# Kernel optimization log

Hardware: AMD Instinct MI355X
Metric: run time of the kernel (lower is better)

The kernel has to match this reference:

```python
import jax, jax.numpy as jnp
import numpy as np

N_NODES = 100000
N_EDGES = 3200000
D_FEAT = 128
HIDDEN = 16
N_CLASSES = 7


def gcn_conv(x, edge_index, edge_weight, W, b, n_nodes):
    h = x @ W  # dense projection first (Fout small)
    src, dst = edge_index[0], edge_index[1]
    # add self-loops with weight 1
    loop = jnp.arange(n_nodes, dtype=edge_index.dtype)
    src_a = jnp.concatenate([src, loop])
    dst_a = jnp.concatenate([dst, loop])
    ew_a = jnp.concatenate([edge_weight, jnp.ones((n_nodes,), dtype=x.dtype)])
    deg = jax.ops.segment_sum(ew_a, dst_a, num_segments=n_nodes)
    dinv = jnp.where(deg > 0, jax.lax.rsqrt(deg), 0.0)
    norm = dinv[src_a] * ew_a * dinv[dst_a]  # [E+N]
    msg = h[src_a] * norm[:, None]  # gather + scale
    out = jax.ops.segment_sum(msg, dst_a, num_segments=n_nodes)
    return out + b


def setup_inputs() -> dict:
    key = jax.random.key(0)
    k = jax.random.split(key, 8)
    x = jax.random.normal(k[0], (N_NODES, D_FEAT), dtype=jnp.float32)
    edge_index = jax.random.randint(k[1], (2, N_EDGES), 0, N_NODES, dtype=jnp.int64)
    edge_weight = jax.random.uniform(k[2], (N_EDGES,), dtype=jnp.float32)
    s1 = 1.0 / np.sqrt(D_FEAT)
    s2 = 1.0 / np.sqrt(HIDDEN)
    W1 = jax.random.uniform(k[3], (D_FEAT, HIDDEN), jnp.float32, -s1, s1)
    b1 = jnp.zeros((HIDDEN,), jnp.float32)
    W2 = jax.random.uniform(k[4], (HIDDEN, N_CLASSES), jnp.float32, -s2, s2)
    b2 = jnp.zeros((N_CLASSES,), jnp.float32)
    return {"x": x, "edge_index": edge_index, "edge_weight": edge_weight,
            "W1": W1, "b1": b1, "W2": W2, "b2": b2}


def reference(x, edge_index, edge_weight, W1, b1, W2, b2):
    h = jax.nn.relu(gcn_conv(x, edge_index, edge_weight, W1, b1, N_NODES))
    out = gcn_conv(h, edge_index, edge_weight, W2, b2, N_NODES)
    return jax.nn.log_softmax(out, axis=1)
```

## Files before the change

### kernel.cpp

```cpp
#include <hip/hip_runtime.h>
#include <hip/hip_fp16.h>
#include <math.h>

constexpr int NN = 100000;
constexpr int NE = 3200000;
constexpr int DF = 128;
constexpr int NH = 16;
constexpr int NC = 7;

constexpr int BN    = 128;
constexpr int NB    = (NN + BN - 1) / BN;
constexpr int CAP   = 4608;
constexpr int CHUNK = 8192;
constexpr int AB    = (NE + CHUNK - 1) / CHUNK;
constexpr int EPT   = CHUNK / 1024;
constexpr int SPT   = (CAP + 1023) / 1024;

constexpr float QS   = 32767.0f;
constexpr float QINV = 1.0f / 32767.0f;

typedef _Float16 half8 __attribute__((ext_vector_type(8)));
typedef float    f32x4 __attribute__((ext_vector_type(4)));

__global__ void k_zero(int* __restrict__ gcur) {
    int t = blockIdx.x * blockDim.x + threadIdx.x;
    if (t < NB) gcur[t] = 0;
}

__global__ void __launch_bounds__(1024)
k_append(const int* __restrict__ src,
         const int* __restrict__ dst,
         const float* __restrict__ w,
         int* __restrict__ gcur,
         uint2* __restrict__ ebuf) {
    __shared__ int hist[NB];
    __shared__ int basev[NB];
    for (int i = threadIdx.x; i < NB; i += 1024) hist[i] = 0;
    __syncthreads();
    int e0 = blockIdx.x * CHUNK;
    unsigned slo[EPT], sw[EPT];
    int sbr[EPT];
#pragma unroll
    for (int k = 0; k < EPT; ++k) {
        int e = e0 + (int)threadIdx.x + k * 1024;
        sbr[k] = -1;
        if (e < NE) {
            int d = __builtin_nontemporal_load(dst + e);
            int b = d >> 7;
            int r = atomicAdd(&hist[b], 1);
            slo[k] = ((unsigned)(d & (BN - 1)) << 17) |
                     (unsigned)__builtin_nontemporal_load(src + e);
            sw[k]  = __float_as_uint(__builtin_nontemporal_load(w + e));
            sbr[k] = (b << 14) | r;
        }
    }
    __syncthreads();
    for (int b = threadIdx.x; b < NB; b += 1024) {
        int c = hist[b];
        basev[b] = (c > 0) ? atomicAdd(&gcur[b], c) : 0;
    }
    __syncthreads();
#pragma unroll
    for (int k = 0; k < EPT; ++k) {
        if (sbr[k] >= 0) {
            int b = sbr[k] >> 14;
            int pos = basev[b] + (sbr[k] & 0x3FFF);
            if (pos < CAP) {
                uint2 v; v.x = slo[k]; v.y = sw[k];
                ebuf[(size_t)b * CAP + pos] = v;
            }
        }
    }
}

__global__ void __launch_bounds__(1024)
k_sort(const int* __restrict__ gcur,
       uint2* __restrict__ ebuf,
       int* __restrict__ rs,
       int* __restrict__ rc,
       float* __restrict__ dinv) {
    __shared__ int cursor[BN];
    __shared__ int scanS[BN];
    __shared__ int startEx[BN];
    __shared__ unsigned sorted[CAP];
    int b = blockIdx.x;
    int tid = threadIdx.x;
    int cnt = min(gcur[b], CAP);
    const uint2* eb = ebuf + (size_t)b * CAP;
    if (tid < BN) cursor[tid] = 0;
    __syncthreads();
    unsigned sval[SPT];
    int sdr[SPT];
#pragma unroll
    for (int k = 0; k < SPT; ++k) {
        int i = tid + k * 1024;
        sdr[k] = -1;
        if (i < cnt) {
            uint2 v = eb[i];
            int dl = (v.x >> 17) & (BN - 1);
            unsigned q = (unsigned)(__uint_as_float(v.y) * QS + 0.5f);
            int r = atomicAdd(&cursor[dl], 1);
            sval[k] = (v.x & 0x1FFFF) | (q << 17);
            sdr[k] = (dl << 13) | r;
        }
    }
    __syncthreads();
    if (tid < BN) scanS[tid] = cursor[tid];
    __syncthreads();
    for (int off = 1; off < BN; off <<= 1) {
        int v = (tid < BN && tid >= off) ? scanS[tid - off] : 0;
        __syncthreads();
        if (tid < BN) scanS[tid] += v;
        __syncthreads();
    }
    if (tid < BN) {
        int ex = scanS[tid] - cursor[tid];
        startEx[tid] = ex;
        int n = b * BN + tid;
        if (n < NN) { rs[n] = b * CAP * 2 + ex; rc[n] = cursor[tid]; }
    }
    __syncthreads();
#pragma unroll
    for (int k = 0; k < SPT; ++k) {
        if (sdr[k] >= 0)
            sorted[startEx[sdr[k] >> 13] + (sdr[k] & 0x1FFF)] = sval[k];
    }
    __syncthreads();
    unsigned* eb32 = (unsigned*)ebuf + (size_t)b * CAP * 2;
    for (int i = tid; i < cnt; i += 1024) eb32[i] = sorted[i];
    if (tid < BN) {
        int n = b * BN + tid;
        if (n < NN) {
            float s = 1.0f;
            int s0 = startEx[tid], c = cursor[tid];
            for (int i = 0; i < c; ++i) s += (float)(sorted[s0 + i] >> 17) * QINV;
            dinv[n] = rsqrtf(s);
        }
    }
}

__global__ void __launch_bounds__(256)
k_proj1(const float* __restrict__ x,
        const float* __restrict__ W1,
        const float* __restrict__ dinv,
        __half* __restrict__ h1p) {
    int wave = threadIdx.x >> 6;
    int lane = threadIdx.x & 63;
    int tile = blockIdx.x * 4 + wave;
    if (tile * 16 >= NN) return;
    int m    = lane & 15;
    int quad = lane >> 4;
    half8 bfrag[4];
#pragma unroll
    for (int kc = 0; kc < 4; ++kc)
#pragma unroll
        for (int j = 0; j < 8; ++j)
            bfrag[kc][j] = (_Float16)W1[(kc * 32 + quad * 8 + j) * NH + m];
    int base = tile * 16;
    const float* xr = x + (size_t)(base + m) * DF + quad * 8;
    f32x4 acc = {0.f, 0.f, 0.f, 0.f};
#pragma unroll
    for (int kc = 0; kc < 4; ++kc) {
        const float4* p = (const float4*)(xr + kc * 32);
        float4 u0 = p[0];
        float4 u1 = p[1];
        half8 afrag;
        afrag[0] = (_Float16)u0.x; afrag[1] = (_Float16)u0.y;
        afrag[2] = (_Float16)u0.z; afrag[3] = (_Float16)u0.w;
        afrag[4] = (_Float16)u1.x; afrag[5] = (_Float16)u1.y;
        afrag[6] = (_Float16)u1.z; afrag[7] = (_Float16)u1.w;
        acc = __builtin_amdgcn_mfma_f32_16x16x32_f16(afrag, bfrag[kc], acc, 0, 0, 0);
    }
    float4 d4 = *(const float4*)(dinv + base + quad * 4);
#pragma unroll
    for (int reg = 0; reg < 4; ++reg) {
        float dd = (reg == 0) ? d4.x : (reg == 1) ? d4.y : (reg == 2) ? d4.z : d4.w;
        int row = quad * 4 + reg;
        h1p[(size_t)(base + row) * 16 + m] = __float2half(acc[reg] * dd);
    }
}

__global__ void __launch_bounds__(1024)
k_agg1p(const int* __restrict__ rs,
        const int* __restrict__ rc,
        const unsigned* __restrict__ cbuf,
        const __half* __restrict__ h1p,
        const float* __restrict__ dinv,
        const float* __restrict__ b1,
        const float* __restrict__ W2,
        __half* __restrict__ h2p) {
    const __half2* hp = (const __half2*)h1p;
    int t = blockIdx.x * 1024 + threadIdx.x;
    int n = t >> 3;
    int f2 = t & 7;
    if (n >= NN) return;
    float2 g0 = __half22float2(hp[n * 8 + f2]);
    float ax = g0.x, ay = g0.y;
    int s0 = rs[n], c = rc[n];
    int i = 0;
    for (; i + 1 < c; i += 2) {
        unsigned e0 = cbuf[s0 + i];
        unsigned e1 = cbuf[s0 + i + 1];
        float2 v0 = __half22float2(hp[(e0 & 0x1FFFF) * 8 + f2]);
        float2 v1 = __half22float2(hp[(e1 & 0x1FFFF) * 8 + f2]);
        float w0 = (float)(e0 >> 17) * QINV;
        float w1 = (float)(e1 >> 17) * QINV;
        ax += w0 * v0.x + w1 * v1.x;
        ay += w0 * v0.y + w1 * v1.y;
    }
    if (i < c) {
        unsigned e0 = cbuf[s0 + i];
        float2 v0 = __half22float2(hp[(e0 & 0x1FFFF) * 8 + f2]);
        float w0 = (float)(e0 >> 17) * QINV;
        ax += w0 * v0.x;
        ay += w0 * v0.y;
    }
    float di = dinv[n];
    float hr0 = fmaxf(di * ax + b1[2 * f2], 0.0f);
    float hr1 = fmaxf(di * ay + b1[2 * f2 + 1], 0.0f);
    float p[NC];
#pragma unroll
    for (int cc = 0; cc < NC; ++cc)
        p[cc] = hr0 * W2[(2 * f2) * NC + cc] + hr1 * W2[(2 * f2 + 1) * NC + cc];
#pragma unroll
    for (int mask = 1; mask < 8; mask <<= 1) {
#pragma unroll
        for (int cc = 0; cc < NC; ++cc)
            p[cc] += __shfl_xor(p[cc], mask, 8);
    }
    float tv = 0.0f;
#pragma unroll
    for (int cc = 0; cc < NC; ++cc)
        if (f2 == cc) tv = p[cc];
    h2p[n * 8 + f2] = __float2half(di * tv);
}

__global__ void __launch_bounds__(1024)
k_agg2_lsm(const int* __restrict__ rs,
           const int* __restrict__ rc,
           const unsigned* __restrict__ cbuf,
           const __half* __restrict__ h2p,
           const float* __restrict__ dinv,
           const float* __restrict__ b2,
           float* __restrict__ out) {
    const __half2* hp = (const __half2*)h2p;
    int t = blockIdx.x * 1024 + threadIdx.x;
    int n = t >> 2;
    int c2 = t & 3;
    if (n >= NN) return;
    float2 g0 = __half22float2(hp[n * 4 + c2]);
    float ax = g0.x, ay = g0.y;
    int s0 = rs[n], c = rc[n];
    int i = 0;
    for (; i + 1 < c; i += 2) {
        unsigned e0 = cbuf[s0 + i];
        unsigned e1 = cbuf[s0 + i + 1];
        float2 v0 = __half22float2(hp[(e0 & 0x1FFFF) * 4 + c2]);
        float2 v1 = __half22float2(hp[(e1 & 0x1FFFF) * 4 + c2]);
        float w0 = (float)(e0 >> 17) * QINV;
        float w1 = (float)(e1 >> 17) * QINV;
        ax += w0 * v0.x + w1 * v1.x;
        ay += w0 * v0.y + w1 * v1.y;
    }
    if (i < c) {
        unsigned e0 = cbuf[s0 + i];
        float2 v0 = __half22float2(hp[(e0 & 0x1FFFF) * 4 + c2]);
        float w0 = (float)(e0 >> 17) * QINV;
        ax += w0 * v0.x;
        ay += w0 * v0.y;
    }
    float di = dinv[n];
    float va = di * ax + b2[2 * c2];
    float vb = (c2 < 3) ? (di * ay + b2[2 * c2 + 1]) : -1e30f;
    float m = fmaxf(va, vb);
#pragma unroll
    for (int mask = 1; mask < 4; mask <<= 1)
        m = fmaxf(m, __shfl_xor(m, mask, 4));
    float s = __expf(va - m) + ((c2 < 3) ? __expf(vb - m) : 0.0f);
#pragma unroll
    for (int mask = 1; mask < 4; mask <<= 1)
        s += __shfl_xor(s, mask, 4);
    float lse = m + __logf(s);
    out[n * NC + 2 * c2] = va - lse;
    if (c2 < 3) out[n * NC + 2 * c2 + 1] = vb - lse;
}

extern "C" void kernel_launch(void* const* d_in, const int* in_sizes, int n_in,
                              void* d_out, int out_size, void* d_ws, size_t ws_size,
                              hipStream_t stream) {
    const float* x  = (const float*)d_in[0];
    const int*   ei = (const int*)d_in[1];
    const float* ew = (const float*)d_in[2];
    const float* W1 = (const float*)d_in[3];
    const float* b1 = (const float*)d_in[4];
    const float* W2 = (const float*)d_in[5];
    const float* b2 = (const float*)d_in[6];
    float* out = (float*)d_out;

    const int* srcp = ei;
    const int* dstp = ei + NE;

    float*  ws   = (float*)d_ws;
    float*  dinv = ws;
    __half* h1p  = (__half*)(ws + 100352);
    __half* h2p  = (__half*)(ws + 900352);
    int*    gcur = (int*)(ws + 1300352);
    int*    rs   = (int*)(ws + 1301376);
    int*    rc   = (int*)(ws + 1401728);
    uint2*  ebuf = (uint2*)(ws + 1502080);
    const unsigned* cbuf = (const unsigned*)ebuf;

    auto cdiv = [](long long a, long long b) { return (int)((a + b - 1) / b); };

    k_zero<<<1, 1024, 0, stream>>>(gcur);
    k_append<<<AB, 1024, 0, stream>>>(srcp, dstp, ew, gcur, ebuf);
    k_sort<<<NB, 1024, 0, stream>>>(gcur, ebuf, rs, rc, dinv);
    k_proj1<<<cdiv(NN, 64), 256, 0, stream>>>(x, W1, dinv, h1p);
    k_agg1p<<<cdiv((long long)NN * 8, 1024), 1024, 0, stream>>>(rs, rc, cbuf, h1p, dinv, b1, W2, h2p);
    k_agg2_lsm<<<cdiv((long long)NN * 4, 1024), 1024, 0, stream>>>(rs, rc, cbuf, h2p, dinv, b2, out);
}
```

Measured before the change: 233.5 us.

## Shard edge-bucket counters into eight segments and shrink append blocks

The append stage now spreads global bucket cursors over eight segment-specific counter arrays, each with its own edge buffer, and uses smaller 256-thread blocks with 2048-edge chunks. The goal is to cut atomic contention on the shared per-bucket cursors and to raise occupancy in the append kernel. The sort kernel gathers all eight segments per bucket and writes the compacted result to a separate buffer instead of writing back in place. In exchange there are four times as many append blocks, each running a per-bucket histogram loop over all buckets. Per-segment capacity limits (640) add overflow truncation risk, and the workspace layout gets larger.

```diff
diff --git a/kernel.cpp b/kernel.cpp
--- a/kernel.cpp
+++ b/kernel.cpp
@@ -10,11 +10,13 @@
 
 constexpr int BN    = 128;
 constexpr int NB    = (NN + BN - 1) / BN;
-constexpr int CAP   = 4608;
-constexpr int CHUNK = 8192;
+constexpr int NSEG  = 8;
+constexpr int CAPS  = 640;
+constexpr int CAPC  = 4608;
+constexpr int SORTW = NSEG * CAPS;
+constexpr int CHUNK = 2048;
 constexpr int AB    = (NE + CHUNK - 1) / CHUNK;
-constexpr int EPT   = CHUNK / 1024;
-constexpr int SPT   = (CAP + 1023) / 1024;
+constexpr int EPT   = CHUNK / 256;
 
 constexpr float QS   = 32767.0f;
 constexpr float QINV = 1.0f / 32767.0f;
@@ -24,25 +26,26 @@
 
 __global__ void k_zero(int* __restrict__ gcur) {
     int t = blockIdx.x * blockDim.x + threadIdx.x;
-    if (t < NB) gcur[t] = 0;
-}
-
-__global__ void __launch_bounds__(1024)
+    if (t < NSEG * 1024) gcur[t] = 0;
+}
+
+__global__ void __launch_bounds__(256)
 k_append(const int* __restrict__ src,
          const int* __restrict__ dst,
          const float* __restrict__ w,
          int* __restrict__ gcur,
-         uint2* __restrict__ ebuf) {
+         uint2* __restrict__ ebufseg) {
     __shared__ int hist[NB];
     __shared__ int basev[NB];
-    for (int i = threadIdx.x; i < NB; i += 1024) hist[i] = 0;
+    for (int i = threadIdx.x; i < NB; i += 256) hist[i] = 0;
     __syncthreads();
     int e0 = blockIdx.x * CHUNK;
+    int seg = blockIdx.x & (NSEG - 1);
     unsigned slo[EPT], sw[EPT];
     int sbr[EPT];
 #pragma unroll
     for (int k = 0; k < EPT; ++k) {
-        int e = e0 + (int)threadIdx.x + k * 1024;
+        int e = e0 + (int)threadIdx.x + k * 256;
         sbr[k] = -1;
         if (e < NE) {
             int d = __builtin_nontemporal_load(dst + e);
@@ -55,9 +58,9 @@
         }
     }
     __syncthreads();
-    for (int b = threadIdx.x; b < NB; b += 1024) {
+    for (int b = threadIdx.x; b < NB; b += 256) {
         int c = hist[b];
-        basev[b] = (c > 0) ? atomicAdd(&gcur[b], c) : 0;
+        basev[b] = (c > 0) ? atomicAdd(&gcur[seg * 1024 + b], c) : 0;
     }
     __syncthreads();
 #pragma unroll
@@ -65,9 +68,9 @@
         if (sbr[k] >= 0) {
             int b = sbr[k] >> 14;
             int pos = basev[b] + (sbr[k] & 0x3FFF);
-            if (pos < CAP) {
+            if (pos < CAPS) {
                 uint2 v; v.x = slo[k]; v.y = sw[k];
-                ebuf[(size_t)b * CAP + pos] = v;
+                ebufseg[(size_t)(seg * NB + b) * CAPS + pos] = v;
             }
         }
     }
@@ -75,33 +78,33 @@
 
 __global__ void __launch_bounds__(1024)
 k_sort(const int* __restrict__ gcur,
-       uint2* __restrict__ ebuf,
+       const uint2* __restrict__ ebufseg,
+       unsigned* __restrict__ cbuf,
        int* __restrict__ rs,
        int* __restrict__ rc,
        float* __restrict__ dinv) {
     __shared__ int cursor[BN];
     __shared__ int scanS[BN];
     __shared__ int startEx[BN];
-    __shared__ unsigned sorted[CAP];
+    __shared__ int scnt[NSEG];
+    __shared__ unsigned sorted[SORTW];
     int b = blockIdx.x;
     int tid = threadIdx.x;
-    int cnt = min(gcur[b], CAP);
-    const uint2* eb = ebuf + (size_t)b * CAP;
     if (tid < BN) cursor[tid] = 0;
-    __syncthreads();
-    unsigned sval[SPT];
-    int sdr[SPT];
-#pragma unroll
-    for (int k = 0; k < SPT; ++k) {
-        int i = tid + k * 1024;
-        sdr[k] = -1;
-        if (i < cnt) {
-            uint2 v = eb[i];
+    if (tid < NSEG) scnt[tid] = min(gcur[tid * 1024 + b], CAPS);
+    __syncthreads();
+    unsigned sval[NSEG];
+    int sdr[NSEG];
+#pragma unroll
+    for (int s = 0; s < NSEG; ++s) {
+        sdr[s] = -1;
+        if (tid < scnt[s]) {
+            uint2 v = ebufseg[(size_t)(s * NB + b) * CAPS + tid];
             int dl = (v.x >> 17) & (BN - 1);
             unsigned q = (unsigned)(__uint_as_float(v.y) * QS + 0.5f);
             int r = atomicAdd(&cursor[dl], 1);
-            sval[k] = (v.x & 0x1FFFF) | (q << 17);
-            sdr[k] = (dl << 13) | r;
+            sval[s] = (v.x & 0x1FFFF) | (q << 17);
+            sdr[s] = (dl << 13) | r;
         }
     }
     __syncthreads();
@@ -117,24 +120,30 @@
         int ex = scanS[tid] - cursor[tid];
         startEx[tid] = ex;
         int n = b * BN + tid;
-        if (n < NN) { rs[n] = b * CAP * 2 + ex; rc[n] = cursor[tid]; }
-    }
-    __syncthreads();
-#pragma unroll
-    for (int k = 0; k < SPT; ++k) {
-        if (sdr[k] >= 0)
-            sorted[startEx[sdr[k] >> 13] + (sdr[k] & 0x1FFF)] = sval[k];
-    }
-    __syncthreads();
-    unsigned* eb32 = (unsigned*)ebuf + (size_t)b * CAP * 2;
-    for (int i = tid; i < cnt; i += 1024) eb32[i] = sorted[i];
+        if (n < NN) {
+            rs[n] = b * CAPC + ex;
+            int c = cursor[tid];
+            if (ex + c > CAPC) c = max(0, CAPC - ex);
+            rc[n] = c;
+        }
+    }
+    __syncthreads();
+#pragma unroll
+    for (int s = 0; s < NSEG; ++s) {
+        if (sdr[s] >= 0)
+            sorted[startEx[sdr[s] >> 13] + (sdr[s] & 0x1FFF)] = sval[s];
+    }
+    __syncthreads();
+    int cnt_tot = scanS[BN - 1];
+    int wlim = min(cnt_tot, CAPC);
+    for (int i = tid; i < wlim; i += 1024) cbuf[(size_t)b * CAPC + i] = sorted[i];
     if (tid < BN) {
         int n = b * BN + tid;
         if (n < NN) {
-            float s = 1.0f;
+            float sum = 1.0f;
             int s0 = startEx[tid], c = cursor[tid];
-            for (int i = 0; i < c; ++i) s += (float)(sorted[s0 + i] >> 17) * QINV;
-            dinv[n] = rsqrtf(s);
+            for (int i = 0; i < c; ++i) sum += (float)(sorted[s0 + i] >> 17) * QINV;
+            dinv[n] = rsqrtf(sum);
         }
     }
 }
@@ -300,21 +309,21 @@
     const int* srcp = ei;
     const int* dstp = ei + NE;
 
-    float*  ws   = (float*)d_ws;
-    float*  dinv = ws;
-    __half* h1p  = (__half*)(ws + 100352);
-    __half* h2p  = (__half*)(ws + 900352);
-    int*    gcur = (int*)(ws + 1300352);
-    int*    rs   = (int*)(ws + 1301376);
-    int*    rc   = (int*)(ws + 1401728);
-    uint2*  ebuf = (uint2*)(ws + 1502080);
-    const unsigned* cbuf = (const unsigned*)ebuf;
+    float*    ws      = (float*)d_ws;
+    float*    dinv    = ws;
+    __half*   h1p     = (__half*)(ws + 100352);
+    __half*   h2p     = (__half*)(ws + 900352);
+    int*      gcur    = (int*)(ws + 1300352);
+    int*      rs      = (int*)(ws + 1308544);
+    int*      rc      = (int*)(ws + 1408896);
+    unsigned* cbuf    = (unsigned*)(ws + 1509248);
+    uint2*    ebufseg = (uint2*)(ws + 5112704);
 
     auto cdiv = [](long long a, long long b) { return (int)((a + b - 1) / b); };
 
-    k_zero<<<1, 1024, 0, stream>>>(gcur);
-    k_append<<<AB, 1024, 0, stream>>>(srcp, dstp, ew, gcur, ebuf);
-    k_sort<<<NB, 1024, 0, stream>>>(gcur, ebuf, rs, rc, dinv);
+    k_zero<<<8, 1024, 0, stream>>>(gcur);
+    k_append<<<AB, 256, 0, stream>>>(srcp, dstp, ew, gcur, ebufseg);
+    k_sort<<<NB, 1024, 0, stream>>>(gcur, ebufseg, cbuf, rs, rc, dinv);
     k_proj1<<<cdiv(NN, 64), 256, 0, stream>>>(x, W1, dinv, h1p);
     k_agg1p<<<cdiv((long long)NN * 8, 1024), 1024, 0, stream>>>(rs, rc, cbuf, h1p, dinv, b1, W2, h2p);
     k_agg2_lsm<<<cdiv((long long)NN * 4, 1024), 1024, 0, stream>>>(rs, rc, cbuf, h2p, dinv, b2, out);
```

Result: slower. 239.3 us (+2.5%).
